# Kernel optimization log

Measured on AMD Instinct MI355X. Metric: run time of the kernel, lower is better.

The kernel has to match this reference:

```python
import jax, jax.numpy as jnp
import numpy as np

HEADS = 8
DIM_HEAD = 64
CHUNK = 128
EPS = 1e-6
KERNEL_EPS = 1e-4


def softmax_kernel(x, proj, is_query):
    # x: [b,h,n,d], proj: [f,d]  (FAVOR+ positive softmax features)
    d = x.shape[-1]
    data_normalizer = d ** -0.25
    ratio = proj.shape[0] ** -0.5
    data_dash = jnp.einsum('bhnd,fd->bhnf', x * data_normalizer, proj)
    diag = 0.5 * (data_normalizer ** 2) * jnp.sum(x * x, axis=-1, keepdims=True)  # [b,h,n,1]
    if is_query:
        m = jnp.max(data_dash, axis=-1, keepdims=True)
    else:
        m = jnp.max(data_dash, axis=(-1, -2), keepdims=True)
    return ratio * (jnp.exp(data_dash - diag - jax.lax.stop_gradient(m)) + KERNEL_EPS)


def infer_hidden_states(q, k, v, chunk_size=CHUNK):
    # q,k: [b,h,n,f], v: [b,h,n,e]; chunked causal linear attention with carried cumsums
    b, h, n, f = q.shape
    e = v.shape[-1]
    nc = n // chunk_size

    def to_chunks(t):
        return jnp.moveaxis(t.reshape(b, h, nc, chunk_size, t.shape[-1]), 2, 0)

    qs, ks, vs = to_chunks(q), to_chunks(k), to_chunks(v)

    def step(carry, inp):
        Z, S = carry  # [b,h,1,f], [b,h,1,f,e]
        qc, kc, vc = inp
        k_cum = Z + jnp.cumsum(kc, axis=2)                       # [b,h,c,f]
        D_inv = 1.0 / jnp.einsum('bhnf,bhnf->bhn', qc, k_cum + EPS)
        ctx = jnp.einsum('bhnf,bhne->bhnfe', kc, vc)             # [b,h,c,f,e]
        ctx_cum = S + jnp.cumsum(ctx, axis=2)
        out = jnp.einsum('bhnfe,bhnf,bhn->bhne', ctx_cum, qc, D_inv)
        return (k_cum[:, :, -1:], ctx_cum[:, :, -1:]), out

    init = (jnp.zeros((b, h, 1, f), q.dtype), jnp.zeros((b, h, 1, f, e), q.dtype))
    (Z, S), outs = jax.lax.scan(step, init, (qs, ks, vs))
    out = jnp.moveaxis(outs, 0, 2).reshape(b, h, n, e)
    return out, Z[:, :, 0], S[:, :, 0]


def reference(x, proj, Wq, Wk, Wv, Wo, bo):
    b, n, dim = x.shape
    h, dh = HEADS, DIM_HEAD

    def split_heads(t):
        return jnp.transpose(t.reshape(b, n, h, dh), (0, 2, 1, 3))

    q = split_heads(x @ Wq)
    k = split_heads(x @ Wk)
    v = split_heads(x @ Wv)

    qf = softmax_kernel(q, proj, is_query=True)
    kf = softmax_kernel(k, proj, is_query=False)

    out, Z, S = infer_hidden_states(qf, kf, v)
    out = jnp.transpose(out, (0, 2, 1, 3)).reshape(b, n, h * dh)
    out = out @ Wo + bo
    return out, Z, S


def setup_inputs() -> dict:
    key = jax.random.key(0)
    ks = jax.random.split(key, 6)
    b, n, dim = 2, 2048, 512
    f = 256
    return {
        'x': jax.random.normal(ks[0], (b, n, dim), jnp.float32),
        'proj': jax.random.normal(ks[1], (f, DIM_HEAD), jnp.float32),
        'Wq': jax.random.normal(ks[2], (dim, dim), jnp.float32) * (dim ** -0.5),
        'Wk': jax.random.normal(ks[3], (dim, dim), jnp.float32) * (dim ** -0.5),
        'Wv': jax.random.normal(ks[4], (dim, dim), jnp.float32) * (dim ** -0.5),
        'Wo': jax.random.normal(ks[5], (dim, dim), jnp.float32) * (dim ** -0.5),
        'bo': jnp.zeros((dim,), jnp.float32),
    }
```

## Files before the change

### kernel.cpp

```cpp
#include <hip/hip_runtime.h>
#include <hip/hip_bf16.h>
#include <math.h>

#define NB    2
#define NSEQ  2048
#define DIMM  512
#define NH    8
#define DHd   64
#define FF    256
#define CHK   128
#define NCHK  16
#define NBH   16

typedef unsigned short ushort_t;
typedef __attribute__((ext_vector_type(8))) __bf16 bf16x8;
typedef __attribute__((ext_vector_type(4))) float floatx4;

__device__ __forceinline__ unsigned short f2bf(float x) {
    union { __hip_bfloat16 h; unsigned short u; } v;
    v.h = __float2bfloat16(x);
    return v.u;
}
__device__ __forceinline__ float bf2f(unsigned short u) {
    union { unsigned short u2[2]; float f; } v;
    v.u2[0] = 0; v.u2[1] = u;
    return v.f;
}
__device__ __forceinline__ unsigned enc_f(float x) {
    unsigned u = __float_as_uint(x);
    return (u & 0x80000000u) ? ~u : (u | 0x80000000u);
}
__device__ __forceinline__ float dec_f(unsigned e) {
    unsigned u = (e & 0x80000000u) ? (e & 0x7fffffffu) : ~e;
    return __uint_as_float(u);
}

__device__ __forceinline__ void gload16(const void* g, void* l) {
    __builtin_amdgcn_global_load_lds(
        (const __attribute__((address_space(1))) void*)g,
        (__attribute__((address_space(3))) void*)l, 16, 0, 0);
}

__device__ __forceinline__ bf16x8 frag8(const ushort_t* lds, int row, int kb) {
    return *((const bf16x8*)lds + row * 8 + (kb ^ (row & 7)));
}
__device__ __forceinline__ bf16x8 fragS(const ushort_t* lds, int row, int kb) {
    return *((const bf16x8*)lds + row * 16 + (kb ^ (row & 15)));
}

__device__ __forceinline__ void stage8(const ushort_t* __restrict__ G, ushort_t* dst,
                                       int ld, int tid) {
#pragma unroll
    for (int t = 0; t < 4; t++) {
        const int g = t * 256 + tid, r = g >> 3, kb = (g & 7) ^ (r & 7);
        gload16(G + (size_t)r * ld + kb * 8, dst + (size_t)g * 8);
    }
}
__device__ __forceinline__ void stage4h(const ushort_t* __restrict__ G, ushort_t* dst,
                                        int ld, int tid) {
#pragma unroll
    for (int t = 0; t < 2; t++) {
        const int g = t * 256 + tid, r = g >> 3, kb = (g & 7) ^ (r & 7);
        gload16(G + (size_t)r * ld + kb * 8, dst + (size_t)g * 8);
    }
}
__device__ __forceinline__ void stageV(const ushort_t* __restrict__ G, ushort_t* dst,
                                       int tid) {
#pragma unroll
    for (int t = 0; t < 4; t++) {
        const int g = t * 256 + tid, r = g >> 4, kb = (g & 15) ^ (r & 15);
        gload16(G + (size_t)r * NSEQ + kb * 8, dst + (size_t)g * 8);
    }
}

__global__ __launch_bounds__(256)
void prep(const float* __restrict__ x, const float* __restrict__ proj,
          const float* __restrict__ W0, const float* __restrict__ W1,
          const float* __restrict__ W2, const float* __restrict__ W3,
          ushort_t* __restrict__ xb, ushort_t* __restrict__ projb,
          ushort_t* __restrict__ T0, ushort_t* __restrict__ T1,
          ushort_t* __restrict__ T2, ushort_t* __restrict__ T3,
          unsigned* __restrict__ mk_u)
{
    __shared__ float t[32][33];
    const int b = blockIdx.x, tid = threadIdx.x;
    if (b < 2048) {
        const int gid = b * 256 + tid;
        const float4 v = *(const float4*)(x + (size_t)gid * 4);
        union { ushort4 v4; unsigned short s[4]; } pk;
        pk.s[0] = f2bf(v.x); pk.s[1] = f2bf(v.y); pk.s[2] = f2bf(v.z); pk.s[3] = f2bf(v.w);
        ((ushort4*)xb)[gid] = pk.v4;
    } else if (b < 2064) {
        const int gid = (b - 2048) * 256 + tid;
        const float dn = 0.35355339059327379f;
        const float4 v = *(const float4*)(proj + (size_t)gid * 4);
        union { ushort4 v4; unsigned short s[4]; } pk;
        pk.s[0] = f2bf(v.x * dn); pk.s[1] = f2bf(v.y * dn);
        pk.s[2] = f2bf(v.z * dn); pk.s[3] = f2bf(v.w * dn);
        ((ushort4*)projb)[gid] = pk.v4;
    } else if (b < 3088) {
        const int idx = b - 2064;
        const int z = idx >> 8, rem = idx & 255;
        const int bx = rem & 15, by = rem >> 4;
        const float* W = (z == 0) ? W0 : (z == 1) ? W1 : (z == 2) ? W2 : W3;
        ushort_t* T = (z == 0) ? T0 : (z == 1) ? T1 : (z == 2) ? T2 : T3;
        const int x0 = bx * 32, y0 = by * 32;
        const int tx = tid & 31, ty = tid >> 5;
#pragma unroll
        for (int i = 0; i < 4; i++)
            t[ty + i * 8][tx] = W[(size_t)(y0 + ty + i * 8) * DIMM + x0 + tx];
        __syncthreads();
#pragma unroll
        for (int i = 0; i < 4; i++)
            T[(size_t)(x0 + ty + i * 8) * DIMM + y0 + tx] = f2bf(t[tx][ty + i * 8]);
    } else {
        if (tid < NBH) mk_u[tid] = 0u;
    }
}

__device__ __forceinline__ void mfma_mainloop(
    const ushort_t* __restrict__ AG, const ushort_t* __restrict__ BG,
    ushort_t* As, ushort_t* Bs, int ldA, int ldB, int K,
    floatx4 acc[4][4], int tid)
{
    const int lane = tid & 63, wid = tid >> 6;
    const int q = lane >> 4, c = lane & 15;
    const int wm = (wid >> 1) * 64, wn = (wid & 1) * 64;

    for (int k0 = 0; k0 < K; k0 += 64) {
#pragma unroll
        for (int t = 0; t < 4; t++) {
            const int g = t * 256 + tid, r = g >> 3, kb = (g & 7) ^ (r & 7);
            gload16(AG + (size_t)r * ldA + k0 + kb * 8, As + (size_t)g * 8);
        }
#pragma unroll
        for (int t = 0; t < 4; t++) {
            const int g = t * 256 + tid, r = g >> 3, kb = (g & 7) ^ (r & 7);
            gload16(BG + (size_t)r * ldB + k0 + kb * 8, Bs + (size_t)g * 8);
        }
        __syncthreads();
#pragma unroll
        for (int ks = 0; ks < 2; ks++) {
            bf16x8 af[4], bfr[4];
#pragma unroll
            for (int i = 0; i < 4; i++) {
                af[i]  = frag8(As, wm + i * 16 + c, ks * 4 + q);
                bfr[i] = frag8(Bs, wn + i * 16 + c, ks * 4 + q);
            }
#pragma unroll
            for (int i = 0; i < 4; i++)
#pragma unroll
                for (int j = 0; j < 4; j++)
                    acc[i][j] = __builtin_amdgcn_mfma_f32_16x16x32_bf16(
                        af[i], bfr[j], acc[i][j], 0, 0, 0);
        }
        __syncthreads();
    }
}

__global__ __launch_bounds__(256)
void gemm_qkv(const ushort_t* __restrict__ xb,
              const ushort_t* __restrict__ Wtq, const ushort_t* __restrict__ Wtk,
              const ushort_t* __restrict__ Wtv, const ushort_t* __restrict__ projb,
              ushort_t* __restrict__ qb, ushort_t* __restrict__ kb,
              ushort_t* __restrict__ vTb, unsigned* __restrict__ mk_u)
{
    __shared__ alignas(16) ushort_t SM[25600];
    __shared__ float red[256];
    ushort_t* As = SM;
    ushort_t* Bs = SM + 8192;
    ushort_t* PS = SM + 17408;
    const int tid = threadIdx.x;
    const int n0 = blockIdx.x * 128, m0 = blockIdx.y * 128, z = blockIdx.z;
    const ushort_t* Bt = (z == 0) ? Wtq : ((z == 1) ? Wtk : Wtv);

    floatx4 zero = {0.f, 0.f, 0.f, 0.f};
    floatx4 acc[4][4];
#pragma unroll
    for (int i = 0; i < 4; i++)
#pragma unroll
        for (int j = 0; j < 4; j++) acc[i][j] = zero;

    mfma_mainloop(xb + (size_t)m0 * DIMM, Bt + (size_t)n0 * DIMM, As, Bs,
                  DIMM, DIMM, DIMM, acc, tid);

    const int lane = tid & 63, wid = tid >> 6;
    const int q = lane >> 4, cl = lane & 15;
    const int wm = (wid >> 1) * 64, wn = (wid & 1) * 64;

#pragma unroll
    for (int i = 0; i < 4; i++)
#pragma unroll
        for (int j = 0; j < 4; j++) {
            const int col = wn + j * 16 + cl;
#pragma unroll
            for (int r = 0; r < 4; r++) {
                const int row = wm + i * 16 + q * 4 + r;
                SM[row * 136 + col] = f2bf(acc[i][j][r]);
            }
        }
    __syncthreads();

    if (z < 2) {
        ushort_t* ob = (z == 0) ? qb : kb;
        if (z == 1) {
#pragma unroll
            for (int t = 0; t < 4; t++) {
                const int g = t * 256 + tid, f = g >> 3, kbg = (g & 7) ^ (f & 7);
                gload16(projb + (size_t)f * 64 + kbg * 8, PS + (size_t)g * 8);
            }
        }
#pragma unroll
        for (int p = 0; p < 16; p++) {
            const int idx = p * 256 + tid;
            const int row = idx >> 5, c4 = idx & 31;
            ushort4 o = *(const ushort4*)&SM[row * 136 + c4 * 4];
            *(ushort4*)(ob + (size_t)(m0 + row) * DIMM + n0 + c4 * 4) = o;
        }
        if (z == 1) {
            const int bb = m0 >> 11;
            const int h0 = n0 >> 6;
            float mx[2] = {-3.0e38f, -3.0e38f};
#pragma unroll
            for (int half = 0; half < 2; half++) {
                __syncthreads();
#pragma unroll
                for (int hh = 0; hh < 2; hh++) {
                    floatx4 a2[4][4];
#pragma unroll
                    for (int i = 0; i < 4; i++)
#pragma unroll
                        for (int j = 0; j < 4; j++) a2[i][j] = zero;
#pragma unroll
                    for (int ks = 0; ks < 2; ks++) {
                        bf16x8 af[4], bfr[4];
#pragma unroll
                        for (int i = 0; i < 4; i++)
                            af[i] = *(const bf16x8*)&SM[(wm + i * 16 + cl) * 136 + hh * 64 + (ks * 4 + q) * 8];
#pragma unroll
                        for (int j = 0; j < 4; j++)
                            bfr[j] = frag8(PS, wn + j * 16 + cl, ks * 4 + q);
#pragma unroll
                        for (int i = 0; i < 4; i++)
#pragma unroll
                            for (int j = 0; j < 4; j++)
                                a2[i][j] = __builtin_amdgcn_mfma_f32_16x16x32_bf16(
                                    af[i], bfr[j], a2[i][j], 0, 0, 0);
                    }
#pragma unroll
                    for (int i = 0; i < 4; i++)
#pragma unroll
                        for (int j = 0; j < 4; j++)
#pragma unroll
                            for (int r = 0; r < 4; r++) mx[hh] = fmaxf(mx[hh], a2[i][j][r]);
                }
                if (half == 0) {
                    __syncthreads();
#pragma unroll
                    for (int t = 0; t < 4; t++) {
                        const int g = t * 256 + tid, f = g >> 3, kbg = (g & 7) ^ (f & 7);
                        gload16(projb + (size_t)(128 + f) * 64 + kbg * 8, PS + (size_t)g * 8);
                    }
                }
            }
#pragma unroll
            for (int hh = 0; hh < 2; hh++) {
                __syncthreads();
                red[tid] = mx[hh];
                __syncthreads();
                for (int s = 128; s > 0; s >>= 1) {
                    if (tid < s) red[tid] = fmaxf(red[tid], red[tid + s]);
                    __syncthreads();
                }
                if (tid == 0) atomicMax(&mk_u[bb * NH + h0 + hh], enc_f(red[0]));
            }
        }
    } else {
        const int bb = m0 >> 11, nbase = m0 & 2047;
#pragma unroll
        for (int p = 0; p < 16; p++) {
            const int idx = p * 256 + tid;
            const int cl2 = idx >> 5, n4 = idx & 31;
            const int C = n0 + cl2;
            const int h = C >> 6, e = C & 63;
            union { ushort4 v4; unsigned short s[4]; } pk;
#pragma unroll
            for (int k = 0; k < 4; k++) pk.s[k] = SM[(n4 * 4 + k) * 136 + cl2];
            *(ushort4*)(vTb + (((size_t)(bb * NH + h) * 64 + e)) * NSEQ + nbase + n4 * 4) = pk.v4;
        }
    }
}

__global__ __launch_bounds__(256)
void gemm_out(const ushort_t* __restrict__ attnb, const ushort_t* __restrict__ Wto,
              float* __restrict__ out, const float* __restrict__ bias)
{
    __shared__ alignas(16) ushort_t As[8192];
    __shared__ alignas(16) ushort_t Bs[8192];
    const int tid = threadIdx.x;
    const int n0 = blockIdx.x * 128, m0 = blockIdx.y * 128;

    floatx4 zero = {0.f, 0.f, 0.f, 0.f};
    floatx4 acc[4][4];
#pragma unroll
    for (int i = 0; i < 4; i++)
#pragma unroll
        for (int j = 0; j < 4; j++) acc[i][j] = zero;

    mfma_mainloop(attnb + (size_t)m0 * DIMM, Wto + (size_t)n0 * DIMM, As, Bs,
                  DIMM, DIMM, DIMM, acc, tid);

    const int lane = tid & 63, wid = tid >> 6;
    const int q = lane >> 4, c = lane & 15;
    const int wm = (wid >> 1) * 64, wn = (wid & 1) * 64;
#pragma unroll
    for (int i = 0; i < 4; i++)
#pragma unroll
        for (int j = 0; j < 4; j++) {
            const int col = n0 + wn + j * 16 + c;
            const float bv = bias[col];
#pragma unroll
            for (int r = 0; r < 4; r++) {
                const int row = m0 + wm + i * 16 + q * 4 + r;
                out[(size_t)row * DIMM + col] = acc[i][j][r] + bv;
            }
        }
}

__global__ __launch_bounds__(256)
void featk(const ushort_t* __restrict__ kb_, const ushort_t* __restrict__ projb,
           const unsigned* __restrict__ mk_u, const ushort_t* __restrict__ vTb,
           ushort_t* __restrict__ kfb, float* __restrict__ CTXT,
           float* __restrict__ Ksum)
{
    __shared__ alignas(16) ushort_t SM[24576];
    __shared__ float dtmp[256];
    __shared__ float diag_l[128];
    __shared__ float colp[2][256];
    ushort_t* As = SM;
    ushort_t* Bs = SM + 8192;
    const int tid = threadIdx.x, lane = tid & 63, wid = tid >> 6;
    const int q = lane >> 4, cl = lane & 15;
    const int m0 = blockIdx.x * 128, h = blockIdx.y;
    const int bb = m0 >> 11, nloc = m0 & 2047;
    const int bh = bb * NH + h;
    const int cidx = nloc >> 7;
    const ushort_t* Aq = kb_ + (size_t)m0 * DIMM + h * 64;

    {
        const int row = tid >> 1, half = tid & 1;
        float s = 0.f;
        const ushort_t* p = Aq + (size_t)row * DIMM + half * 32;
#pragma unroll
        for (int d = 0; d < 32; d += 4) {
            ushort4 w = *(const ushort4*)(p + d);
            float a = bf2f(w.x), b2 = bf2f(w.y), c2 = bf2f(w.z), d2 = bf2f(w.w);
            s += a * a + b2 * b2 + c2 * c2 + d2 * d2;
        }
        dtmp[tid] = s;
    }
    __syncthreads();
    if (tid < 128) diag_l[tid] = (dtmp[2 * tid] + dtmp[2 * tid + 1]) * 0.0625f;

#pragma unroll
    for (int t = 0; t < 4; t++) {
        const int g = t * 256 + tid, r = g >> 3, kb = (g & 7) ^ (r & 7);
        gload16(Aq + (size_t)r * DIMM + kb * 8, As + (size_t)g * 8);
    }
#pragma unroll
    for (int t = 0; t < 8; t++) {
        const int g = t * 256 + tid, r = g >> 3, kb = (g & 7) ^ (r & 7);
        gload16(projb + (size_t)r * 64 + kb * 8, Bs + (size_t)g * 8);
    }
    __syncthreads();

    floatx4 zero = {0.f, 0.f, 0.f, 0.f};
    floatx4 acc[4][8];
#pragma unroll
    for (int i = 0; i < 4; i++)
#pragma unroll
        for (int j = 0; j < 8; j++) acc[i][j] = zero;
    const int wm = (wid >> 1) * 64, wn = (wid & 1) * 128;
#pragma unroll
    for (int ks = 0; ks < 2; ks++) {
        bf16x8 af[4], bfr[8];
#pragma unroll
        for (int i = 0; i < 4; i++) af[i] = frag8(As, wm + i * 16 + cl, ks * 4 + q);
#pragma unroll
        for (int j = 0; j < 8; j++) bfr[j] = frag8(Bs, wn + j * 16 + cl, ks * 4 + q);
#pragma unroll
        for (int i = 0; i < 4; i++)
#pragma unroll
            for (int j = 0; j < 8; j++)
                acc[i][j] = __builtin_amdgcn_mfma_f32_16x16x32_bf16(
                    af[i], bfr[j], acc[i][j], 0, 0, 0);
    }
    __syncthreads();

    const float mk = dec_f(mk_u[bh]);
#pragma unroll
    for (int i = 0; i < 4; i++)
#pragma unroll
        for (int r = 0; r < 4; r++) {
            const int row = wm + i * 16 + q * 4 + r;
            const float cc = diag_l[row] + mk;
#pragma unroll
            for (int j = 0; j < 8; j++)
                acc[i][j][r] = 0.0625f * (__expf(acc[i][j][r] - cc) + 1.0e-4f);
        }

#pragma unroll
    for (int j = 0; j < 8; j++) {
        float s = 0.f;
#pragma unroll
        for (int i = 0; i < 4; i++)
            s += acc[i][j][0] + acc[i][j][1] + acc[i][j][2] + acc[i][j][3];
        s += __shfl_xor(s, 16);
        s += __shfl_xor(s, 32);
        if (q == 0) colp[wid >> 1][wn + j * 16 + cl] = s;
    }

    const size_t frow = (size_t)bh * NSEQ + nloc;
#pragma unroll
    for (int hf = 0; hf < 2; hf++) {
        __syncthreads();
        if ((wid & 1) == hf) {
#pragma unroll
            for (int i = 0; i < 4; i++)
#pragma unroll
                for (int j = 0; j < 8; j++) {
                    const int col = j * 16 + cl;
#pragma unroll
                    for (int r = 0; r < 4; r++) {
                        const int row = wm + i * 16 + q * 4 + r;
                        SM[row * 132 + col] = f2bf(acc[i][j][r]);
                    }
                }
        }
        if (hf == 0) {
            Ksum[((size_t)bh * NCHK + cidx) * FF + tid] = colp[0][tid] + colp[1][tid];
        }
        __syncthreads();
#pragma unroll
        for (int p = 0; p < 16; p++) {
            const int idx = p * 256 + tid;
            const int row = idx >> 5, c4 = idx & 31;
            ushort4 o = *(const ushort4*)&SM[row * 132 + c4 * 4];
            *(ushort4*)(kfb + (frow + row) * FF + hf * 128 + c4 * 4) = o;
        }
    }

    __syncthreads();
    ushort_t* Vs = SM;
    ushort_t* T  = SM + 8192;
    const ushort_t* Vg = vTb + ((size_t)bh * 64) * NSEQ + nloc;
#pragma unroll
    for (int t = 0; t < 4; t++) {
        const int g = t * 256 + tid, r = g >> 4, kb = (g & 15) ^ (r & 15);
        gload16(Vg + (size_t)r * NSEQ + kb * 8, Vs + (size_t)g * 8);
    }

    const size_t cbase = ((size_t)bh * NCHK + cidx) * 64;
#pragma unroll
    for (int fq = 0; fq < 4; fq++) {
        if ((wid & 1) == (fq >> 1)) {
#pragma unroll
            for (int jj = 0; jj < 4; jj++) {
                const int j = (fq & 1) * 4 + jj;
#pragma unroll
                for (int i = 0; i < 4; i++)
#pragma unroll
                    for (int r = 0; r < 4; r++) {
                        const int n = wm + i * 16 + q * 4 + r;
                        T[(jj * 16 + cl) * 136 + n] = f2bf(acc[i][j][r]);
                    }
            }
        }
        __syncthreads();
        floatx4 accc[4];
#pragma unroll
        for (int jj = 0; jj < 4; jj++) accc[jj] = zero;
#pragma unroll
        for (int kt = 0; kt < 4; kt++) {
            const bf16x8 av = fragS(Vs, wid * 16 + cl, kt * 4 + q);
#pragma unroll
            for (int jj = 0; jj < 4; jj++) {
                const bf16x8 bv = *(const bf16x8*)(T + (jj * 16 + cl) * 136 + (kt * 4 + q) * 8);
                accc[jj] = __builtin_amdgcn_mfma_f32_16x16x32_bf16(av, bv, accc[jj], 0, 0, 0);
            }
        }
#pragma unroll
        for (int jj = 0; jj < 4; jj++) {
            const int f = fq * 64 + jj * 16 + cl;
#pragma unroll
            for (int r = 0; r < 4; r++) {
                const int e = wid * 16 + q * 4 + r;
                CTXT[(cbase + e) * FF + f] = accc[jj][r];
            }
        }
        __syncthreads();
    }
}

__global__ void prefix_zs(float* __restrict__ Ksum, float* __restrict__ Zout,
                          const float* __restrict__ CTXT, ushort_t* __restrict__ ctxp,
                          float* __restrict__ Sout)
{
    const int b = blockIdx.x;
    if (b < 1024) {
        const int idx = b * 256 + threadIdx.x;
        const int bh = idx >> 14, ef = idx & 16383;
        const int e = ef >> 8, f = ef & 255;
        float run = 0.f;
#pragma unroll
        for (int c = 0; c < NCHK; c++) {
            const size_t o = (((size_t)bh * NCHK + c) * 64 + e) * FF + f;
            const float t = CTXT[o];
            ctxp[o] = f2bf(run);
            run += t;
        }
        Sout[((size_t)bh * FF + f) * 64 + e] = run;
    } else {
        const int idx = (b - 1024) * 256 + threadIdx.x;
        const int bh = idx >> 8, f = idx & 255;
        float run = 0.f;
#pragma unroll
        for (int c = 0; c < NCHK; c++) {
            const size_t o = ((size_t)(bh * NCHK + c)) * FF + f;
            const float t = Ksum[o];
            Ksum[o] = run;
            run += t;
        }
        Zout[(size_t)bh * FF + f] = run;
    }
}

__device__ __forceinline__ void st1_step(const ushort_t* QFs, const ushort_t* Bk,
                                         floatx4 acc1[8], int wv, int cl, int q)
{
#pragma unroll
    for (int ks = 0; ks < 2; ks++) {
        const bf16x8 af = frag8(QFs, wv * 16 + cl, ks * 4 + q);
        bf16x8 bfr[8];
#pragma unroll
        for (int j = 0; j < 8; j++) bfr[j] = frag8(Bk, j * 16 + cl, ks * 4 + q);
#pragma unroll
        for (int j = 0; j < 8; j++)
            acc1[j] = __builtin_amdgcn_mfma_f32_16x16x32_bf16(af, bfr[j], acc1[j], 0, 0, 0);
    }
}

__device__ __forceinline__ void pv4(const ushort_t* CpB, const ushort_t* QFs,
                                    floatx4 acc2[4], int wv, int cl, int q)
{
#pragma unroll
    for (int ks = 0; ks < 2; ks++) {
        const bf16x8 bfr = frag8(QFs, wv * 16 + cl, ks * 4 + q);
#pragma unroll
        for (int i = 0; i < 4; i++) {
            const bf16x8 af = frag8(CpB, i * 16 + cl, ks * 4 + q);
            acc2[i] = __builtin_amdgcn_mfma_f32_16x16x32_bf16(af, bfr, acc2[i], 0, 0, 0);
        }
    }
}

__global__ __launch_bounds__(256)
void chunk_out_half(const ushort_t* __restrict__ qb_, const ushort_t* __restrict__ projb,
                    const ushort_t* __restrict__ kfb, const ushort_t* __restrict__ vTb,
                    const float* __restrict__ Zex, const ushort_t* __restrict__ ctxp,
                    ushort_t* __restrict__ attnb)
{
    __shared__ alignas(16) ushort_t QF[16384];
    __shared__ alignas(16) ushort_t BufA[8192];
    __shared__ alignas(16) ushort_t Ssl[8192];
    __shared__ alignas(16) ushort_t BufB[4096];
    __shared__ float zeps[256];
    __shared__ float dtmp[256];
    __shared__ float diag_l[64];
    __shared__ float rows_part[64];
    __shared__ float denp[256];
    __shared__ float den_l[64];

    const int tid = threadIdx.x, lane = tid & 63, wv = tid >> 6;
    const int q = lane >> 4, cl = lane & 15;
    const int bh = blockIdx.x >> 5, r5 = blockIdx.x & 31;
    const int c = r5 >> 1, hq = r5 & 1;
    const int bb = bh >> 3, h = bh & 7;
    const int n0 = c * CHK, q0 = n0 + hq * 64;
    const ushort_t* Kf = kfb + ((size_t)bh * NSEQ + n0) * FF;
    const ushort_t* Aq = qb_ + ((size_t)(bb * NSEQ + q0)) * DIMM + h * 64;
    const ushort_t* Vt = vTb + ((size_t)bh * 64) * NSEQ + n0;
    const ushort_t* Cp = ctxp + ((size_t)bh * NCHK + c) * 64 * FF;

    zeps[tid] = Zex[((size_t)bh * NCHK + c) * FF + tid] + 1.0e-6f;

    stage4h(Aq, BufB, DIMM, tid);
    stage8(projb, BufA, 64, tid);
    stage8(projb + 128 * 64, Ssl, 64, tid);
    {
        const int row = tid >> 2, qd = tid & 3;
        float s = 0.f;
        const ushort_t* p = Aq + (size_t)row * DIMM + qd * 16;
#pragma unroll
        for (int d = 0; d < 16; d += 4) {
            ushort4 w = *(const ushort4*)(p + d);
            float a = bf2f(w.x), b2 = bf2f(w.y), c2 = bf2f(w.z), d2 = bf2f(w.w);
            s += a * a + b2 * b2 + c2 * c2 + d2 * d2;
        }
        dtmp[tid] = s;
    }
    __syncthreads();
    if (tid < 64)
        diag_l[tid] = (dtmp[4 * tid] + dtmp[4 * tid + 1] +
                       dtmp[4 * tid + 2] + dtmp[4 * tid + 3]) * 0.0625f;

    floatx4 zero = {0.f, 0.f, 0.f, 0.f};
    floatx4 accqA[8], accqB[8];
#pragma unroll
    for (int j = 0; j < 8; j++) { accqA[j] = zero; accqB[j] = zero; }
#pragma unroll
    for (int ks = 0; ks < 2; ks++) {
        const bf16x8 af = frag8(BufB, wv * 16 + cl, ks * 4 + q);
#pragma unroll
        for (int j = 0; j < 8; j++) {
            const bf16x8 b0 = frag8(BufA, j * 16 + cl, ks * 4 + q);
            accqA[j] = __builtin_amdgcn_mfma_f32_16x16x32_bf16(af, b0, accqA[j], 0, 0, 0);
        }
#pragma unroll
        for (int j = 0; j < 8; j++) {
            const bf16x8 b1 = frag8(Ssl, j * 16 + cl, ks * 4 + q);
            accqB[j] = __builtin_amdgcn_mfma_f32_16x16x32_bf16(af, b1, accqB[j], 0, 0, 0);
        }
    }
    float rmax[4];
#pragma unroll
    for (int r = 0; r < 4; r++) {
        float m = -3.0e38f;
#pragma unroll
        for (int j = 0; j < 8; j++) m = fmaxf(m, fmaxf(accqA[j][r], accqB[j][r]));
        m = fmaxf(m, __shfl_xor(m, 1)); m = fmaxf(m, __shfl_xor(m, 2));
        m = fmaxf(m, __shfl_xor(m, 4)); m = fmaxf(m, __shfl_xor(m, 8));
        rmax[r] = m;
    }
    __syncthreads();
#pragma unroll
    for (int r = 0; r < 4; r++) {
        const int rowL = wv * 16 + q * 4 + r;
        const float cc = diag_l[rowL] + rmax[r];
#pragma unroll
        for (int j = 0; j < 8; j++) {
            {
                const int col = j * 16 + cl;
                const float v = 0.0625f * (__expf(accqA[j][r] - cc) + 1.0e-4f);
                const int s = col >> 6, fp = col & 63;
                QF[s * 4096 + (rowL * 8 + ((fp >> 3) ^ (rowL & 7))) * 8 + (fp & 7)] = f2bf(v);
            }
            {
                const int col = 128 + j * 16 + cl;
                const float v = 0.0625f * (__expf(accqB[j][r] - cc) + 1.0e-4f);
                const int s = col >> 6, fp = col & 63;
                QF[s * 4096 + (rowL * 8 + ((fp >> 3) ^ (rowL & 7))) * 8 + (fp & 7)] = f2bf(v);
            }
        }
    }
    stage8(Kf, Ssl, FF, tid);
    __syncthreads();

    floatx4 acc1[8];
#pragma unroll
    for (int j = 0; j < 8; j++) acc1[j] = zero;
    stage8(Kf + 64, BufA, FF, tid);
    st1_step(QF, Ssl, acc1, wv, cl, q);
    __syncthreads();
    stage8(Kf + 128, Ssl, FF, tid);
    st1_step(QF + 4096, BufA, acc1, wv, cl, q);
    __syncthreads();
    stage8(Kf + 192, BufA, FF, tid);
    st1_step(QF + 8192, Ssl, acc1, wv, cl, q);
    __syncthreads();
    st1_step(QF + 12288, BufA, acc1, wv, cl, q);

    const int rbase = hq * 64;
#pragma unroll
    for (int r = 0; r < 4; r++) {
        const int rowL = wv * 16 + q * 4 + r;
        const int rowG = rbase + rowL;
        float part = 0.f;
#pragma unroll
        for (int j = 0; j < 8; j++) {
            const int col = j * 16 + cl;
            const float v = (col <= rowG) ? acc1[j][r] : 0.f;
            part += v;
            Ssl[(rowL * 16 + ((col >> 3) ^ (rowL & 15))) * 8 + (col & 7)] = f2bf(v);
        }
        part += __shfl_xor(part, 1); part += __shfl_xor(part, 2);
        part += __shfl_xor(part, 4); part += __shfl_xor(part, 8);
        if (cl == 0) rows_part[rowL] = part;
    }
    __syncthreads();

    stageV(Vt, BufA, tid);
    stage4h(Cp, BufB, FF, tid);
    float dacc = 0.f;
    {
        const int drow = tid >> 2, dq = tid & 3;
        const ushort_t* QQ = QF + dq * 4096;
#pragma unroll
        for (int gi = 0; gi < 8; gi++) {
            const ushort_t* gp = QQ + ((size_t)drow * 8 + (gi ^ (drow & 7))) * 8;
            const int kbase = dq * 64 + gi * 8;
#pragma unroll
            for (int e2 = 0; e2 < 8; e2++)
                dacc = fmaf(bf2f(gp[e2]), zeps[kbase + e2], dacc);
        }
    }
    __syncthreads();

    floatx4 acc2[4];
#pragma unroll
    for (int i = 0; i < 4; i++) acc2[i] = zero;
#pragma unroll
    for (int kk = 0; kk < 4; kk++) {
        const bf16x8 bfr = fragS(Ssl, wv * 16 + cl, kk * 4 + q);
#pragma unroll
        for (int i = 0; i < 4; i++) {
            const bf16x8 af = fragS(BufA, i * 16 + cl, kk * 4 + q);
            acc2[i] = __builtin_amdgcn_mfma_f32_16x16x32_bf16(af, bfr, acc2[i], 0, 0, 0);
        }
    }
    denp[tid] = dacc;
    __syncthreads();

    stage4h(Cp + 64, BufA, FF, tid);
    stage4h(Cp + 128, BufA + 4096, FF, tid);
    pv4(BufB, QF, acc2, wv, cl, q);
    __syncthreads();
    stage4h(Cp + 192, BufB, FF, tid);
    pv4(BufA, QF + 4096, acc2, wv, cl, q);
    pv4(BufA + 4096, QF + 8192, acc2, wv, cl, q);
    if (tid < 64)
        den_l[tid] = rows_part[tid] + denp[4 * tid] + denp[4 * tid + 1] +
                     denp[4 * tid + 2] + denp[4 * tid + 3];
    __syncthreads();
    pv4(BufB, QF + 12288, acc2, wv, cl, q);

    const float dinv = 1.0f / den_l[wv * 16 + cl];
#pragma unroll
    for (int i = 0; i < 4; i++)
#pragma unroll
        for (int r = 0; r < 4; r++) {
            const int e = i * 16 + q * 4 + r;
            Ssl[(wv * 16 + cl) * 68 + e] = f2bf(acc2[i][r] * dinv);
        }
    __syncthreads();
#pragma unroll
    for (int p = 0; p < 4; p++) {
        const int idx = p * 256 + tid;
        const int row = idx >> 4, e4 = idx & 15;
        ushort4 o = *(const ushort4*)&Ssl[row * 68 + e4 * 4];
        *(ushort4*)(attnb + ((size_t)(bb * NSEQ + q0 + row)) * DIMM + h * 64 + e4 * 4) = o;
    }
}

extern "C" void kernel_launch(void* const* d_in, const int* in_sizes, int n_in,
                              void* d_out, int out_size, void* d_ws, size_t ws_size,
                              hipStream_t stream)
{
    (void)in_sizes; (void)n_in; (void)out_size; (void)ws_size;
    const float* x    = (const float*)d_in[0];
    const float* proj = (const float*)d_in[1];
    const float* Wq   = (const float*)d_in[2];
    const float* Wk   = (const float*)d_in[3];
    const float* Wv   = (const float*)d_in[4];
    const float* Wo   = (const float*)d_in[5];
    const float* bo   = (const float*)d_in[6];
    float* out = (float*)d_out;

    char* W = (char*)d_ws;
    float*    CTXT = (float*)W;              W += (size_t)16777216;
    ushort_t* kfb  = (ushort_t*)W;           W += (size_t)16777216;
    ushort_t* ctxp = (ushort_t*)W;           W += (size_t)8388608;
    ushort_t* qb   = (ushort_t*)W;           W += (size_t)4194304;
    ushort_t* kb   = (ushort_t*)W;           W += (size_t)4194304;
    ushort_t* xb   = (ushort_t*)W;           W += (size_t)4194304;
    ushort_t* vTb  = (ushort_t*)W;           W += (size_t)4194304;
    ushort_t* Wtq  = (ushort_t*)W;           W += (size_t)524288;
    ushort_t* Wtk  = (ushort_t*)W;           W += (size_t)524288;
    ushort_t* Wtv  = (ushort_t*)W;           W += (size_t)524288;
    ushort_t* Wto  = (ushort_t*)W;           W += (size_t)524288;
    ushort_t* projb = (ushort_t*)W;          W += (size_t)32768;
    float*    Ksum = (float*)W;              W += (size_t)262144;
    unsigned* mk_u = (unsigned*)W;           W += (size_t)256;

    ushort_t* attnb = xb;

    float* Zout = out + (size_t)4096 * 512;
    float* Sout = Zout + (size_t)NBH * FF;

    hipLaunchKernelGGL(prep, dim3(3089), dim3(256), 0, stream,
                       x, proj, Wq, Wk, Wv, Wo, xb, projb, Wtq, Wtk, Wtv, Wto, mk_u);
    hipLaunchKernelGGL(gemm_qkv, dim3(4, 32, 3), dim3(256), 0, stream,
                       xb, Wtq, Wtk, Wtv, projb, qb, kb, vTb, mk_u);
    hipLaunchKernelGGL(featk, dim3(32, 8), dim3(256), 0, stream,
                       kb, projb, mk_u, vTb, kfb, CTXT, Ksum);
    hipLaunchKernelGGL(prefix_zs, dim3(1040), dim3(256), 0, stream,
                       Ksum, Zout, CTXT, ctxp, Sout);
    hipLaunchKernelGGL(chunk_out_half, dim3(512), dim3(256), 0, stream,
                       qb, projb, kfb, vTb, Ksum, ctxp, attnb);
    hipLaunchKernelGGL(gemm_out, dim3(4, 32), dim3(256), 0, stream, attnb, Wto, out, bo);
}
```

Measured before the change: 144.2 us.

## Split featk over feature halves, shrink gemm_out tiles, reorder gemm_qkv block mapping

featk now launches twice as many blocks, each handling 128 of the 256 random features. It also stages V into its own shared buffer up front, so those loads overlap the projection GEMM. gemm_out uses 64-row tiles to double its block count, and gemm_qkv flattens its grid so the Q/K/V blocks for the same tile are interleaved. The goal is more waves in flight on the many CUs. The cost is recomputing the row norms and reloading the K and V tiles per feature half, plus smaller per-block MFMA work.

```diff
diff --git a/kernel.cpp b/kernel.cpp
--- a/kernel.cpp
+++ b/kernel.cpp
@@ -171,7 +171,9 @@
     ushort_t* Bs = SM + 8192;
     ushort_t* PS = SM + 17408;
     const int tid = threadIdx.x;
-    const int n0 = blockIdx.x * 128, m0 = blockIdx.y * 128, z = blockIdx.z;
+    const int bid = blockIdx.x;
+    const int z = bid % 3, tt = bid / 3;
+    const int n0 = (tt & 3) * 128, m0 = (tt >> 2) * 128;
     const ushort_t* Bt = (z == 0) ? Wtq : ((z == 1) ? Wtk : Wtv);
 
     floatx4 zero = {0.f, 0.f, 0.f, 0.f};
@@ -295,26 +297,47 @@
 void gemm_out(const ushort_t* __restrict__ attnb, const ushort_t* __restrict__ Wto,
               float* __restrict__ out, const float* __restrict__ bias)
 {
-    __shared__ alignas(16) ushort_t As[8192];
+    __shared__ alignas(16) ushort_t As[4096];
     __shared__ alignas(16) ushort_t Bs[8192];
     const int tid = threadIdx.x;
-    const int n0 = blockIdx.x * 128, m0 = blockIdx.y * 128;
+    const int n0 = blockIdx.x * 128, m0 = blockIdx.y * 64;
+    const ushort_t* AG = attnb + (size_t)m0 * DIMM;
+    const ushort_t* BG = Wto + (size_t)n0 * DIMM;
 
     floatx4 zero = {0.f, 0.f, 0.f, 0.f};
-    floatx4 acc[4][4];
-#pragma unroll
-    for (int i = 0; i < 4; i++)
+    floatx4 acc[2][4];
+#pragma unroll
+    for (int i = 0; i < 2; i++)
 #pragma unroll
         for (int j = 0; j < 4; j++) acc[i][j] = zero;
-
-    mfma_mainloop(attnb + (size_t)m0 * DIMM, Wto + (size_t)n0 * DIMM, As, Bs,
-                  DIMM, DIMM, DIMM, acc, tid);
 
     const int lane = tid & 63, wid = tid >> 6;
     const int q = lane >> 4, c = lane & 15;
-    const int wm = (wid >> 1) * 64, wn = (wid & 1) * 64;
-#pragma unroll
-    for (int i = 0; i < 4; i++)
+    const int wm = (wid >> 1) * 32, wn = (wid & 1) * 64;
+
+    for (int k0 = 0; k0 < DIMM; k0 += 64) {
+        stage4h(AG + k0, As, DIMM, tid);
+        stage8(BG + k0, Bs, DIMM, tid);
+        __syncthreads();
+#pragma unroll
+        for (int ks = 0; ks < 2; ks++) {
+            bf16x8 af[2], bfr[4];
+#pragma unroll
+            for (int i = 0; i < 2; i++) af[i] = frag8(As, wm + i * 16 + c, ks * 4 + q);
+#pragma unroll
+            for (int j = 0; j < 4; j++) bfr[j] = frag8(Bs, wn + j * 16 + c, ks * 4 + q);
+#pragma unroll
+            for (int i = 0; i < 2; i++)
+#pragma unroll
+                for (int j = 0; j < 4; j++)
+                    acc[i][j] = __builtin_amdgcn_mfma_f32_16x16x32_bf16(
+                        af[i], bfr[j], acc[i][j], 0, 0, 0);
+        }
+        __syncthreads();
+    }
+
+#pragma unroll
+    for (int i = 0; i < 2; i++)
 #pragma unroll
         for (int j = 0; j < 4; j++) {
             const int col = n0 + wn + j * 16 + c;
@@ -333,19 +356,22 @@
            ushort_t* __restrict__ kfb, float* __restrict__ CTXT,
            float* __restrict__ Ksum)
 {
-    __shared__ alignas(16) ushort_t SM[24576];
+    __shared__ alignas(16) ushort_t SM[17408];
+    __shared__ alignas(16) ushort_t Vs[8192];
     __shared__ float dtmp[256];
     __shared__ float diag_l[128];
-    __shared__ float colp[2][256];
+    __shared__ float colp[2][128];
     ushort_t* As = SM;
     ushort_t* Bs = SM + 8192;
     const int tid = threadIdx.x, lane = tid & 63, wid = tid >> 6;
     const int q = lane >> 4, cl = lane & 15;
-    const int m0 = blockIdx.x * 128, h = blockIdx.y;
+    const int m0 = blockIdx.x * 128, h = blockIdx.y, fh = blockIdx.z;
     const int bb = m0 >> 11, nloc = m0 & 2047;
     const int bh = bb * NH + h;
     const int cidx = nloc >> 7;
     const ushort_t* Aq = kb_ + (size_t)m0 * DIMM + h * 64;
+    const ushort_t* Vg = vTb + ((size_t)bh * 64) * NSEQ + nloc;
+    const ushort_t* Pj = projb + (size_t)fh * 128 * 64;
 
     {
         const int row = tid >> 1, half = tid & 1;
@@ -359,39 +385,30 @@
         }
         dtmp[tid] = s;
     }
+    stage8(Aq, As, DIMM, tid);
+    stage8(Pj, Bs, 64, tid);
+    stageV(Vg, Vs, tid);
     __syncthreads();
     if (tid < 128) diag_l[tid] = (dtmp[2 * tid] + dtmp[2 * tid + 1]) * 0.0625f;
 
-#pragma unroll
-    for (int t = 0; t < 4; t++) {
-        const int g = t * 256 + tid, r = g >> 3, kb = (g & 7) ^ (r & 7);
-        gload16(Aq + (size_t)r * DIMM + kb * 8, As + (size_t)g * 8);
-    }
-#pragma unroll
-    for (int t = 0; t < 8; t++) {
-        const int g = t * 256 + tid, r = g >> 3, kb = (g & 7) ^ (r & 7);
-        gload16(projb + (size_t)r * 64 + kb * 8, Bs + (size_t)g * 8);
-    }
-    __syncthreads();
-
     floatx4 zero = {0.f, 0.f, 0.f, 0.f};
-    floatx4 acc[4][8];
+    floatx4 acc[4][4];
 #pragma unroll
     for (int i = 0; i < 4; i++)
 #pragma unroll
-        for (int j = 0; j < 8; j++) acc[i][j] = zero;
-    const int wm = (wid >> 1) * 64, wn = (wid & 1) * 128;
+        for (int j = 0; j < 4; j++) acc[i][j] = zero;
+    const int wm = (wid >> 1) * 64, wn = (wid & 1) * 64;
 #pragma unroll
     for (int ks = 0; ks < 2; ks++) {
-        bf16x8 af[4], bfr[8];
+        bf16x8 af[4], bfr[4];
 #pragma unroll
         for (int i = 0; i < 4; i++) af[i] = frag8(As, wm + i * 16 + cl, ks * 4 + q);
 #pragma unroll
-        for (int j = 0; j < 8; j++) bfr[j] = frag8(Bs, wn + j * 16 + cl, ks * 4 + q);
+        for (int j = 0; j < 4; j++) bfr[j] = frag8(Bs, wn + j * 16 + cl, ks * 4 + q);
 #pragma unroll
         for (int i = 0; i < 4; i++)
 #pragma unroll
-            for (int j = 0; j < 8; j++)
+            for (int j = 0; j < 4; j++)
                 acc[i][j] = __builtin_amdgcn_mfma_f32_16x16x32_bf16(
                     af[i], bfr[j], acc[i][j], 0, 0, 0);
     }
@@ -405,12 +422,12 @@
             const int row = wm + i * 16 + q * 4 + r;
             const float cc = diag_l[row] + mk;
 #pragma unroll
-            for (int j = 0; j < 8; j++)
+            for (int j = 0; j < 4; j++)
                 acc[i][j][r] = 0.0625f * (__expf(acc[i][j][r] - cc) + 1.0e-4f);
         }
 
 #pragma unroll
-    for (int j = 0; j < 8; j++) {
+    for (int j = 0; j < 4; j++) {
         float s = 0.f;
 #pragma unroll
         for (int i = 0; i < 4; i++)
@@ -420,59 +437,45 @@
         if (q == 0) colp[wid >> 1][wn + j * 16 + cl] = s;
     }
 
+#pragma unroll
+    for (int i = 0; i < 4; i++)
+#pragma unroll
+        for (int j = 0; j < 4; j++) {
+            const int col = wn + j * 16 + cl;
+#pragma unroll
+            for (int r = 0; r < 4; r++) {
+                const int row = wm + i * 16 + q * 4 + r;
+                SM[row * 136 + col] = f2bf(acc[i][j][r]);
+            }
+        }
+    __syncthreads();
+
+    if (tid < 128)
+        Ksum[((size_t)bh * NCHK + cidx) * FF + fh * 128 + tid] = colp[0][tid] + colp[1][tid];
+
     const size_t frow = (size_t)bh * NSEQ + nloc;
 #pragma unroll
-    for (int hf = 0; hf < 2; hf++) {
-        __syncthreads();
-        if ((wid & 1) == hf) {
-#pragma unroll
-            for (int i = 0; i < 4; i++)
-#pragma unroll
-                for (int j = 0; j < 8; j++) {
-                    const int col = j * 16 + cl;
-#pragma unroll
-                    for (int r = 0; r < 4; r++) {
-                        const int row = wm + i * 16 + q * 4 + r;
-                        SM[row * 132 + col] = f2bf(acc[i][j][r]);
-                    }
-                }
-        }
-        if (hf == 0) {
-            Ksum[((size_t)bh * NCHK + cidx) * FF + tid] = colp[0][tid] + colp[1][tid];
-        }
-        __syncthreads();
-#pragma unroll
-        for (int p = 0; p < 16; p++) {
-            const int idx = p * 256 + tid;
-            const int row = idx >> 5, c4 = idx & 31;
-            ushort4 o = *(const ushort4*)&SM[row * 132 + c4 * 4];
-            *(ushort4*)(kfb + (frow + row) * FF + hf * 128 + c4 * 4) = o;
-        }
-    }
-
-    __syncthreads();
-    ushort_t* Vs = SM;
-    ushort_t* T  = SM + 8192;
-    const ushort_t* Vg = vTb + ((size_t)bh * 64) * NSEQ + nloc;
-#pragma unroll
-    for (int t = 0; t < 4; t++) {
-        const int g = t * 256 + tid, r = g >> 4, kb = (g & 15) ^ (r & 15);
-        gload16(Vg + (size_t)r * NSEQ + kb * 8, Vs + (size_t)g * 8);
-    }
-
+    for (int p = 0; p < 16; p++) {
+        const int idx = p * 256 + tid;
+        const int row = idx >> 5, c4 = idx & 31;
+        ushort4 o = *(const ushort4*)&SM[row * 136 + c4 * 4];
+        *(ushort4*)(kfb + (frow + row) * FF + fh * 128 + c4 * 4) = o;
+    }
+    __syncthreads();
+
+    ushort_t* T = SM;
     const size_t cbase = ((size_t)bh * NCHK + cidx) * 64;
 #pragma unroll
-    for (int fq = 0; fq < 4; fq++) {
-        if ((wid & 1) == (fq >> 1)) {
+    for (int fq = 0; fq < 2; fq++) {
+        if ((wid & 1) == fq) {
 #pragma unroll
             for (int jj = 0; jj < 4; jj++) {
-                const int j = (fq & 1) * 4 + jj;
 #pragma unroll
                 for (int i = 0; i < 4; i++)
 #pragma unroll
                     for (int r = 0; r < 4; r++) {
                         const int n = wm + i * 16 + q * 4 + r;
-                        T[(jj * 16 + cl) * 136 + n] = f2bf(acc[i][j][r]);
+                        T[(jj * 16 + cl) * 136 + n] = f2bf(acc[i][jj][r]);
                     }
             }
         }
@@ -491,7 +494,7 @@
         }
 #pragma unroll
         for (int jj = 0; jj < 4; jj++) {
-            const int f = fq * 64 + jj * 16 + cl;
+            const int f = fh * 128 + fq * 64 + jj * 16 + cl;
 #pragma unroll
             for (int r = 0; r < 4; r++) {
                 const int e = wid * 16 + q * 4 + r;
@@ -799,13 +802,13 @@
 
     hipLaunchKernelGGL(prep, dim3(3089), dim3(256), 0, stream,
                        x, proj, Wq, Wk, Wv, Wo, xb, projb, Wtq, Wtk, Wtv, Wto, mk_u);
-    hipLaunchKernelGGL(gemm_qkv, dim3(4, 32, 3), dim3(256), 0, stream,
+    hipLaunchKernelGGL(gemm_qkv, dim3(384), dim3(256), 0, stream,
                        xb, Wtq, Wtk, Wtv, projb, qb, kb, vTb, mk_u);
-    hipLaunchKernelGGL(featk, dim3(32, 8), dim3(256), 0, stream,
+    hipLaunchKernelGGL(featk, dim3(32, 8, 2), dim3(256), 0, stream,
                        kb, projb, mk_u, vTb, kfb, CTXT, Ksum);
     hipLaunchKernelGGL(prefix_zs, dim3(1040), dim3(256), 0, stream,
                        Ksum, Zout, CTXT, ctxp, Sout);
     hipLaunchKernelGGL(chunk_out_half, dim3(512), dim3(256), 0, stream,
                        qb, projb, kfb, vTb, Ksum, ctxp, attnb);
-    hipLaunchKernelGGL(gemm_out, dim3(4, 32), dim3(256), 0, stream, attnb, Wto, out, bo);
-}
+    hipLaunchKernelGGL(gemm_out, dim3(4, 64), dim3(256), 0, stream, attnb, Wto, out, bo);
+}
```

After: 136.6 us. 1.06x faster.
